# Kernel optimization log

Hardware: AMD Instinct MI355X
Metric: run time of the kernel (lower is better)

Reference implementation:

```python
import jax, jax.numpy as jnp
import numpy as np

EMB_DIM = 1024
ATTN_DIM = 1024


def setup_inputs() -> dict:
    key = jax.random.key(0)
    k_x, k_wk, k_wq, k_wv = jax.random.split(key, 4)
    bound = 1.0 / np.sqrt(EMB_DIM)  # nn.Linear default init range
    return {
        "embedded": jax.random.normal(k_x, (4, 2048, EMB_DIM), dtype=jnp.float32),
        "W_k": jax.random.uniform(k_wk, (ATTN_DIM, EMB_DIM), jnp.float32, -bound, bound),
        "W_q": jax.random.uniform(k_wq, (ATTN_DIM, EMB_DIM), jnp.float32, -bound, bound),
        "W_v": jax.random.uniform(k_wv, (ATTN_DIM, EMB_DIM), jnp.float32, -bound, bound),
    }


def reference(embedded, W_k, W_q, W_v):
    # Linear (bias=False): y = x @ W.T
    K = jnp.einsum("bse,ae->bsa", embedded, W_k)
    Q = jnp.einsum("bse,ae->bsa", embedded, W_q)
    V = jnp.einsum("bse,ae->bsa", embedded, W_v)
    S = K.shape[1]
    scale = 1.0 / jnp.sqrt(jnp.float32(ATTN_DIM))
    scores = jnp.einsum("bqa,bka->bqk", Q, K) * scale  # [B, S, S]
    causal = jnp.tril(jnp.ones((S, S), dtype=bool))  # True = keep
    scores = jnp.where(causal[None, :, :], scores, -jnp.inf)
    attn = jax.nn.softmax(scores, axis=2)
    out = jnp.einsum("bqk,bka->bqa", attn, V)
    # torch.round(x, decimals=4)
    return jnp.round(out * 1e4) / 1e4
```

## Files before the change

### kernel.cpp

```cpp
#include <hip/hip_runtime.h>
#include <stdint.h>

#define B_ 4
#define S_ 2048
#define E_ 1024
#define D_ 1024

typedef short  bf16x8 __attribute__((ext_vector_type(8)));
typedef float  f32x4  __attribute__((ext_vector_type(4)));

static __device__ __forceinline__ unsigned short f2bf(float f) {
    unsigned int u = __float_as_uint(f);
    u += 0x7fffu + ((u >> 16) & 1u);
    return (unsigned short)(u >> 16);
}

static __device__ __forceinline__ void async16(const unsigned short* g, unsigned short* l) {
    auto gp = (const __attribute__((address_space(1))) void*)(uintptr_t)g;
    auto lp = (__attribute__((address_space(3))) void*)(uintptr_t)l;
    __builtin_amdgcn_global_load_lds(gp, lp, 16, 0, 0);
}


__global__ __launch_bounds__(256)
void convert_kernel(const float* __restrict__ x,  const float* __restrict__ Wk,
                    const float* __restrict__ Wq, const float* __restrict__ Wv,
                    unsigned short* __restrict__ xb, unsigned short* __restrict__ Wb)
{
    const long long total  = (long long)B_ * S_ * E_ + 3LL * D_ * E_;
    const long long stride = (long long)gridDim.x * 256 * 4;
    for (long long idx = ((long long)blockIdx.x * 256 + threadIdx.x) * 4;
         idx < total; idx += stride) {
        const float* src; unsigned short* dst; long long off;
        if (idx < (long long)B_ * S_ * E_) {
            src = x; dst = xb; off = idx;
        } else {
            long long w = idx - (long long)B_ * S_ * E_;
            const int sel = (int)(w >> 20);
            off = w & 1048575LL;
            src = (sel == 0) ? Wk : (sel == 1) ? Wq : Wv;
            dst = Wb + ((long long)sel << 20);
        }
        const float4 f = *(const float4*)(src + off);
        ushort4 u = { f2bf(f.x), f2bf(f.y), f2bf(f.z), f2bf(f.w) };
        *(ushort4*)(dst + off) = u;
    }
}

__global__ __launch_bounds__(512, 2)
void proj_kernel(const unsigned short* __restrict__ xb,
                 const unsigned short* __restrict__ Wb,
                 unsigned short* __restrict__ Qb,
                 unsigned short* __restrict__ Kb,
                 unsigned short* __restrict__ Vt)
{
    extern __shared__ __align__(16) unsigned short lds[];

    const int bid = blockIdx.x;
    const int swz = (bid & 7) * 48 + (bid >> 3);
    const int my  = swz / 12;
    const int ny  = swz - my * 12;
    const int m0  = my * 256;
    const int wsel = ny >> 2;
    const int nloc = (ny & 3) * 256;

    const int t = threadIdx.x;
    const int lane = t & 63, wave = t >> 6;
    const int l15 = lane & 15, quad = lane >> 4;
    const int wm2 = wave & 1, wn4 = wave >> 1;
    const int lr = lane >> 3;
    const int lc = ((lane & 7) ^ lr) * 8;
    const int l7 = l15 & 7;

    const unsigned short* gAb = xb + (size_t)(m0 + lr) * E_ + lc;
    const unsigned short* gBb = Wb + (size_t)(ny * 256 + lr) * E_ + lc;

    f32x4 acc[8][4];
    #pragma unroll
    for (int i = 0; i < 8; i++)
        #pragma unroll
        for (int j = 0; j < 4; j++) acc[i][j] = {0.f, 0.f, 0.f, 0.f};

    #pragma unroll
    for (int i = 0; i < 8; i++) {
        const int u = wave * 8 + i;
        if (u < 32) async16(gAb + (size_t)(u * 8) * E_,        lds +         u * 512);
        else        async16(gBb + (size_t)((u - 32) * 8) * E_, lds + 32768 + (u - 32) * 512);
    }
    __syncthreads();

    for (int kt = 0; kt < 16; kt++) {
        const int c = kt & 1;
        const unsigned short* Ac = lds + c * 16384;
        const unsigned short* Bc = lds + 32768 + c * 16384;
        unsigned short* An = lds + (c ^ 1) * 16384;
        unsigned short* Bn = lds + 32768 + (c ^ 1) * 16384;

        #pragma unroll
        for (int p = 0; p < 4; p++) {
            if (kt < 15) {
                const int k0 = (kt + 1) * 64;
                #pragma unroll
                for (int i = 0; i < 2; i++) {
                    const int u = wave * 8 + p * 2 + i;
                    if (u < 32) async16(gAb + (size_t)(u * 8) * E_ + k0,        An +        u * 512);
                    else        async16(gBb + (size_t)((u - 32) * 8) * E_ + k0, Bn + (u - 32) * 512);
                }
            }
            const int mh = p >> 1, nh = p & 1;
            bf16x8 af[2][4], bfr[2][2];
            #pragma unroll
            for (int s = 0; s < 2; s++) {
                const int cs = ((s * 4 + quad) ^ l7) * 8;
                #pragma unroll
                for (int ii = 0; ii < 4; ii++) {
                    const int r = wm2 * 128 + (mh * 4 + ii) * 16 + l15;
                    af[s][ii] = *(const bf16x8*)&Ac[r * 64 + cs];
                }
                #pragma unroll
                for (int jj = 0; jj < 2; jj++) {
                    const int r = wn4 * 64 + (nh * 2 + jj) * 16 + l15;
                    bfr[s][jj] = *(const bf16x8*)&Bc[r * 64 + cs];
                }
            }
            __builtin_amdgcn_s_setprio(1);
            #pragma unroll
            for (int s = 0; s < 2; s++)
                #pragma unroll
                for (int ii = 0; ii < 4; ii++)
                    #pragma unroll
                    for (int jj = 0; jj < 2; jj++)
                        acc[mh * 4 + ii][nh * 2 + jj] =
                            __builtin_amdgcn_mfma_f32_16x16x32_bf16(
                                af[s][ii], bfr[s][jj], acc[mh * 4 + ii][nh * 2 + jj], 0, 0, 0);
            __builtin_amdgcn_s_setprio(0);
            if (p < 3) __builtin_amdgcn_s_barrier();
        }
        __syncthreads();
    }

    if (wsel == 0) {
        #pragma unroll
        for (int i = 0; i < 8; i++)
            #pragma unroll
            for (int j = 0; j < 4; j++) {
                const int gn = nloc + wn4 * 64 + j * 16 + l15;
                #pragma unroll
                for (int r = 0; r < 4; r++) {
                    const int gm = m0 + wm2 * 128 + i * 16 + quad * 4 + r;
                    Kb[(size_t)gm * D_ + gn] = f2bf(acc[i][j][r]);
                }
            }
    } else if (wsel == 1) {
        #pragma unroll
        for (int i = 0; i < 8; i++)
            #pragma unroll
            for (int j = 0; j < 4; j++) {
                const int gn = nloc + wn4 * 64 + j * 16 + l15;
                #pragma unroll
                for (int r = 0; r < 4; r++) {
                    const int gm = m0 + wm2 * 128 + i * 16 + quad * 4 + r;
                    Qb[(size_t)gm * D_ + gn] = f2bf(acc[i][j][r] * 0.03125f);
                }
            }
    } else {
        #pragma unroll
        for (int i = 0; i < 8; i++)
            #pragma unroll
            for (int j = 0; j < 4; j++) {
                const int s0 = m0 + wm2 * 128 + i * 16 + quad * 4;
                const int b  = s0 >> 11, sl = s0 & (S_ - 1);
                const int gn = nloc + wn4 * 64 + j * 16 + l15;
                ushort4 u = { f2bf(acc[i][j][0]), f2bf(acc[i][j][1]),
                              f2bf(acc[i][j][2]), f2bf(acc[i][j][3]) };
                *(ushort4*)&Vt[((size_t)(b << 10) + gn) * S_ + sl] = u;
            }
    }
}

__global__ __launch_bounds__(256, 4)
void expscores_kernel(const unsigned short* __restrict__ Qb,
                      const unsigned short* __restrict__ Kb,
                      unsigned short* __restrict__ P,
                      float* __restrict__ rowpart)
{
    int rem = blockIdx.x;
    int mt = 15, cnt = 16;
    while (rem >= cnt) { rem -= cnt; mt--; cnt--; }
    const int nt = rem;
    const int b  = blockIdx.y;

    __shared__ __align__(16) unsigned short As[128 * 64];
    __shared__ __align__(16) unsigned short Bs[128 * 64];

    const int t = threadIdx.x;
    const int m0 = mt * 128, n0 = nt * 128;

    const int lane = t & 63, wave = t >> 6;
    const int l15 = lane & 15, quad = lane >> 4;
    const int wm = wave & 1, wn = wave >> 1;
    const int sr = lane >> 3;
    const int sq = ((lane & 7) ^ sr) * 8;
    const int l7 = l15 & 7;

    const unsigned short* gA = Qb + (size_t)b * S_ * D_ + (size_t)(m0 + wave * 32 + sr) * D_ + sq;
    const unsigned short* gB = Kb + (size_t)b * S_ * D_ + (size_t)(n0 + wave * 32 + sr) * D_ + sq;
    unsigned short* lA = &As[wave * 2048];
    unsigned short* lB = &Bs[wave * 2048];

    f32x4 acc[4][4];
    #pragma unroll
    for (int i = 0; i < 4; i++)
        #pragma unroll
        for (int j = 0; j < 4; j++) acc[i][j] = {0.f, 0.f, 0.f, 0.f};

    for (int kt = 0; kt < 16; kt++) {
        const int k0 = kt * 64;
        __syncthreads();
        #pragma unroll
        for (int i = 0; i < 4; i++) {
            async16(gA + k0 + i * 8 * D_, lA + i * 512);
            async16(gB + k0 + i * 8 * D_, lB + i * 512);
        }
        __syncthreads();

        #pragma unroll
        for (int s = 0; s < 2; s++) {
            const int cs = ((s * 4 + quad) ^ l7) * 8;
            bf16x8 af[4], bfr[4];
            #pragma unroll
            for (int i = 0; i < 4; i++)
                af[i] = *(const bf16x8*)&As[(wm * 64 + i * 16 + l15) * 64 + cs];
            #pragma unroll
            for (int j = 0; j < 4; j++)
                bfr[j] = *(const bf16x8*)&Bs[(wn * 64 + j * 16 + l15) * 64 + cs];
            #pragma unroll
            for (int i = 0; i < 4; i++)
                #pragma unroll
                for (int j = 0; j < 4; j++)
                    acc[i][j] = __builtin_amdgcn_mfma_f32_16x16x32_bf16(af[i], bfr[j], acc[i][j], 0, 0, 0);
        }
    }

    unsigned short* Pb = P + (size_t)b * S_ * S_;
    #pragma unroll
    for (int i = 0; i < 4; i++)
        #pragma unroll
        for (int j = 0; j < 4; j++) {
            const int gn = n0 + wn * 64 + j * 16 + l15;
            #pragma unroll
            for (int r = 0; r < 4; r++) {
                const int gm = m0 + wm * 64 + i * 16 + quad * 4 + r;
                const float e = (gn <= gm) ? __expf(acc[i][j][r]) : 0.f;
                acc[i][j][r] = e;
                Pb[(size_t)gm * S_ + gn] = f2bf(e);
            }
        }

    float* rp = rowpart + ((size_t)b * 32 + nt * 2 + wn) * S_;
    #pragma unroll
    for (int i = 0; i < 4; i++) {
        float rsub[4];
        #pragma unroll
        for (int r = 0; r < 4; r++) {
            float s = acc[i][0][r] + acc[i][1][r] + acc[i][2][r] + acc[i][3][r];
            #pragma unroll
            for (int off = 8; off; off >>= 1) s += __shfl_xor(s, off);
            rsub[r] = s;
        }
        if (l15 == 0) {
            #pragma unroll
            for (int r = 0; r < 4; r++)
                rp[m0 + wm * 64 + i * 16 + quad * 4 + r] = rsub[r];
        }
    }
}

__global__ __launch_bounds__(256, 2)
void pv_kernel(const unsigned short* __restrict__ P,
               const unsigned short* __restrict__ Vt,
               const float* __restrict__ rowpart,
               float* __restrict__ out)
{
    const int nt = blockIdx.x;
    const int yy = blockIdx.y;
    const int b  = blockIdx.z;
    const int mt = (b & 2) ? yy : (15 - yy);

    __shared__ __align__(16) unsigned short As[2 * 128 * 64];
    __shared__ __align__(16) unsigned short Bs[2 * 128 * 64];

    const int t = threadIdx.x;
    const int m0 = mt * 128, n0 = nt * 128;
    const int niter = 2 * mt + 2;

    const int lane = t & 63, wave = t >> 6;
    const int l15 = lane & 15, quad = lane >> 4;
    const int wm = wave & 1, wn = wave >> 1;
    const int sr = lane >> 3;
    const int sq = ((lane & 7) ^ sr) * 8;
    const int l7 = l15 & 7;

    const unsigned short* gA = P  + (size_t)b * S_ * S_ + (size_t)(m0 + wave * 32 + sr) * S_ + sq;
    const unsigned short* gB = Vt + (size_t)b * D_ * S_ + (size_t)(n0 + wave * 32 + sr) * S_ + sq;
    unsigned short* lA = &As[wave * 2048];
    unsigned short* lB = &Bs[wave * 2048];

    const float* rp = rowpart + (size_t)b * 32 * S_ + (m0 + wm * 64 + lane);
    float rsum = 0.f;
    for (int k = 0; k < niter; k++) rsum += rp[(size_t)k * S_];
    const float invr = 1.0f / rsum;

    f32x4 acc[4][4];
    #pragma unroll
    for (int i = 0; i < 4; i++)
        #pragma unroll
        for (int j = 0; j < 4; j++) acc[i][j] = {0.f, 0.f, 0.f, 0.f};

    #pragma unroll
    for (int i = 0; i < 4; i++) {
        async16(gA + i * 8 * S_, lA + i * 512);
        async16(gB + i * 8 * S_, lB + i * 512);
    }

    int buf = 0;
    for (int kt = 0; kt < niter; kt++) {
        __syncthreads();
        if (kt + 1 < niter) {
            const int k0 = (kt + 1) * 64;
            const int nb = (buf ^ 1) * 8192;
            #pragma unroll
            for (int i = 0; i < 4; i++) {
                async16(gA + k0 + i * 8 * S_, lA + nb + i * 512);
                async16(gB + k0 + i * 8 * S_, lB + nb + i * 512);
            }
        }
        const unsigned short* Ac = As + buf * 8192;
        const unsigned short* Bc = Bs + buf * 8192;
        #pragma unroll
        for (int s = 0; s < 2; s++) {
            const int cs = ((s * 4 + quad) ^ l7) * 8;
            bf16x8 af[4], bfr[4];
            #pragma unroll
            for (int i = 0; i < 4; i++)
                af[i] = *(const bf16x8*)&Ac[(wm * 64 + i * 16 + l15) * 64 + cs];
            #pragma unroll
            for (int j = 0; j < 4; j++)
                bfr[j] = *(const bf16x8*)&Bc[(wn * 64 + j * 16 + l15) * 64 + cs];
            #pragma unroll
            for (int i = 0; i < 4; i++)
                #pragma unroll
                for (int j = 0; j < 4; j++)
                    acc[i][j] = __builtin_amdgcn_mfma_f32_16x16x32_bf16(af[i], bfr[j], acc[i][j], 0, 0, 0);
        }
        buf ^= 1;
    }

    #pragma unroll
    for (int i = 0; i < 4; i++) {
        #pragma unroll
        for (int r = 0; r < 4; r++) {
            const float vr = __shfl(invr, i * 16 + quad * 4 + r);
            const int gm = m0 + wm * 64 + i * 16 + quad * 4 + r;
            #pragma unroll
            for (int j = 0; j < 4; j++) {
                const int gn = n0 + wn * 64 + j * 16 + l15;
                out[((size_t)b * S_ + gm) * D_ + gn] = rintf(acc[i][j][r] * vr * 1e4f) * 1e-4f;
            }
        }
    }
}

extern "C" void kernel_launch(void* const* d_in, const int* in_sizes, int n_in,
                              void* d_out, int out_size, void* d_ws, size_t ws_size,
                              hipStream_t stream)
{
    (void)in_sizes; (void)n_in; (void)out_size; (void)ws_size;
    const float* x  = (const float*)d_in[0];
    const float* Wk = (const float*)d_in[1];
    const float* Wq = (const float*)d_in[2];
    const float* Wv = (const float*)d_in[3];
    float* out = (float*)d_out;

    char* ws = (char*)d_ws;
    unsigned short* Qb = (unsigned short*)ws;
    unsigned short* Kb = Qb + (size_t)B_ * S_ * D_;
    unsigned short* Vt = Kb + (size_t)B_ * S_ * D_;
    unsigned short* P  = Vt + (size_t)B_ * D_ * S_;
    unsigned short* xb = P;
    unsigned short* Wb = xb + (size_t)B_ * S_ * E_;
    float* rowpart = (float*)(P + (size_t)B_ * S_ * S_);

    convert_kernel  <<<2048, 256, 0, stream>>>(x, Wk, Wq, Wv, xb, Wb);
    proj_kernel     <<<dim3(384, 1, 1), 512, 131072, stream>>>(xb, Wb, Qb, Kb, Vt);
    expscores_kernel<<<dim3(136, B_, 1), 256, 0, stream>>>(Qb, Kb, P, rowpart);
    pv_kernel       <<<dim3(8, 16, B_),  256, 0, stream>>>(P, Vt, rowpart, out);
}
```

Measured before the change: 238.1 us.

## Restructure QKV projection GEMM into 256x128 tiles with triple-buffered async loads

Result: faster. 229.5 us (-3.6%).

```diff
diff --git a/kernel.cpp b/kernel.cpp
--- a/kernel.cpp
+++ b/kernel.cpp
@@ -57,12 +57,12 @@
     extern __shared__ __align__(16) unsigned short lds[];
 
     const int bid = blockIdx.x;
-    const int swz = (bid & 7) * 48 + (bid >> 3);
-    const int my  = swz / 12;
-    const int ny  = swz - my * 12;
-    const int m0  = my * 256;
-    const int wsel = ny >> 2;
-    const int nloc = (ny & 3) * 256;
+    const int xcd = bid & 7, ii = bid >> 3;
+    const int my = xcd * 4 + ii / 24;
+    const int ny = ii % 24;
+    const int m0 = my * 256;
+    const int wsel = ny >> 3;
+    const int nloc = (ny & 7) * 128;
 
     const int t = threadIdx.x;
     const int lane = t & 63, wave = t >> 6;
@@ -72,107 +72,136 @@
     const int lc = ((lane & 7) ^ lr) * 8;
     const int l7 = l15 & 7;
 
-    const unsigned short* gAb = xb + (size_t)(m0 + lr) * E_ + lc;
-    const unsigned short* gBb = Wb + (size_t)(ny * 256 + lr) * E_ + lc;
-
-    f32x4 acc[8][4];
+    const unsigned short* gA = xb + (size_t)(m0 + lr) * E_ + lc;
+    const unsigned short* gB = Wb + (size_t)(ny * 128 + lr) * E_ + lc;
+    const int uA = wave * 4;
+    const int uB = wave * 2;
+
+    f32x4 acc[8][2];
     #pragma unroll
     for (int i = 0; i < 8; i++)
         #pragma unroll
-        for (int j = 0; j < 4; j++) acc[i][j] = {0.f, 0.f, 0.f, 0.f};
-
-    #pragma unroll
-    for (int i = 0; i < 8; i++) {
-        const int u = wave * 8 + i;
-        if (u < 32) async16(gAb + (size_t)(u * 8) * E_,        lds +         u * 512);
-        else        async16(gBb + (size_t)((u - 32) * 8) * E_, lds + 32768 + (u - 32) * 512);
-    }
-    __syncthreads();
-
+        for (int j = 0; j < 2; j++) acc[i][j] = {0.f, 0.f, 0.f, 0.f};
+
+    #pragma unroll
+    for (int j = 0; j < 4; j++) async16(gA + (size_t)((uA + j) * 8) * E_, lds + (uA + j) * 512);
+    #pragma unroll
+    for (int j = 0; j < 2; j++) async16(gB + (size_t)((uB + j) * 8) * E_, lds + 49152 + (uB + j) * 512);
+    #pragma unroll
+    for (int j = 0; j < 4; j++) async16(gA + (size_t)((uA + j) * 8) * E_ + 64, lds + 16384 + (uA + j) * 512);
+    #pragma unroll
+    for (int j = 0; j < 2; j++) async16(gB + (size_t)((uB + j) * 8) * E_ + 64, lds + 49152 + 8192 + (uB + j) * 512);
+    asm volatile("s_waitcnt vmcnt(6)" ::: "memory");
+    __builtin_amdgcn_s_barrier();
+
+    int cbuf = 0;
     for (int kt = 0; kt < 16; kt++) {
-        const int c = kt & 1;
-        const unsigned short* Ac = lds + c * 16384;
-        const unsigned short* Bc = lds + 32768 + c * 16384;
-        unsigned short* An = lds + (c ^ 1) * 16384;
-        unsigned short* Bn = lds + 32768 + (c ^ 1) * 16384;
-
-        #pragma unroll
-        for (int p = 0; p < 4; p++) {
-            if (kt < 15) {
-                const int k0 = (kt + 1) * 64;
-                #pragma unroll
-                for (int i = 0; i < 2; i++) {
-                    const int u = wave * 8 + p * 2 + i;
-                    if (u < 32) async16(gAb + (size_t)(u * 8) * E_ + k0,        An +        u * 512);
-                    else        async16(gBb + (size_t)((u - 32) * 8) * E_ + k0, Bn + (u - 32) * 512);
+        const unsigned short* Ac = lds + cbuf * 16384;
+        const unsigned short* Bc = lds + 49152 + cbuf * 8192;
+        const int sbuf = (cbuf >= 1) ? (cbuf - 1) : 2;
+        unsigned short* An = lds + sbuf * 16384;
+        unsigned short* Bn = lds + 49152 + sbuf * 8192;
+        const int k0n = (kt + 2) * 64;
+        const bool st = (kt < 14);
+
+        if (st) {
+            async16(gA + (size_t)((uA + 0) * 8) * E_ + k0n, An + (uA + 0) * 512);
+            async16(gA + (size_t)((uA + 1) * 8) * E_ + k0n, An + (uA + 1) * 512);
+            async16(gA + (size_t)((uA + 2) * 8) * E_ + k0n, An + (uA + 2) * 512);
+        }
+        bf16x8 af[4][2], bfv[2][2];
+        #pragma unroll
+        for (int s = 0; s < 2; s++) {
+            const int cs = ((s * 4 + quad) ^ l7) * 8;
+            #pragma unroll
+            for (int mf = 0; mf < 4; mf++)
+                af[mf][s] = *(const bf16x8*)&Ac[(wm2 * 128 + mf * 16 + l15) * 64 + cs];
+            #pragma unroll
+            for (int nf = 0; nf < 2; nf++)
+                bfv[nf][s] = *(const bf16x8*)&Bc[(wn4 * 32 + nf * 16 + l15) * 64 + cs];
+        }
+        __builtin_amdgcn_s_barrier();
+        asm volatile("s_waitcnt lgkmcnt(0)" ::: "memory");
+        __builtin_amdgcn_sched_barrier(0);
+        __builtin_amdgcn_s_setprio(1);
+        #pragma unroll
+        for (int s = 0; s < 2; s++)
+            #pragma unroll
+            for (int mf = 0; mf < 4; mf++)
+                #pragma unroll
+                for (int nf = 0; nf < 2; nf++)
+                    acc[mf][nf] = __builtin_amdgcn_mfma_f32_16x16x32_bf16(
+                        af[mf][s], bfv[nf][s], acc[mf][nf], 0, 0, 0);
+        __builtin_amdgcn_s_setprio(0);
+        __builtin_amdgcn_s_barrier();
+
+        if (st) {
+            async16(gA + (size_t)((uA + 3) * 8) * E_ + k0n, An + (uA + 3) * 512);
+            async16(gB + (size_t)((uB + 0) * 8) * E_ + k0n, Bn + (uB + 0) * 512);
+            async16(gB + (size_t)((uB + 1) * 8) * E_ + k0n, Bn + (uB + 1) * 512);
+        }
+        bf16x8 ag[4][2];
+        #pragma unroll
+        for (int s = 0; s < 2; s++) {
+            const int cs = ((s * 4 + quad) ^ l7) * 8;
+            #pragma unroll
+            for (int mf = 0; mf < 4; mf++)
+                ag[mf][s] = *(const bf16x8*)&Ac[(wm2 * 128 + (4 + mf) * 16 + l15) * 64 + cs];
+        }
+        __builtin_amdgcn_s_barrier();
+        asm volatile("s_waitcnt lgkmcnt(0)" ::: "memory");
+        __builtin_amdgcn_sched_barrier(0);
+        __builtin_amdgcn_s_setprio(1);
+        #pragma unroll
+        for (int s = 0; s < 2; s++)
+            #pragma unroll
+            for (int mf = 0; mf < 4; mf++)
+                #pragma unroll
+                for (int nf = 0; nf < 2; nf++)
+                    acc[4 + mf][nf] = __builtin_amdgcn_mfma_f32_16x16x32_bf16(
+                        ag[mf][s], bfv[nf][s], acc[4 + mf][nf], 0, 0, 0);
+        __builtin_amdgcn_s_setprio(0);
+
+        if (st) asm volatile("s_waitcnt vmcnt(6)" ::: "memory");
+        else    asm volatile("s_waitcnt vmcnt(0)" ::: "memory");
+        __builtin_amdgcn_s_barrier();
+        cbuf = (cbuf >= 2) ? 0 : cbuf + 1;
+    }
+
+    if (wsel == 0) {
+        #pragma unroll
+        for (int mf = 0; mf < 8; mf++)
+            #pragma unroll
+            for (int nf = 0; nf < 2; nf++) {
+                const int gn = nloc + wn4 * 32 + nf * 16 + l15;
+                #pragma unroll
+                for (int r = 0; r < 4; r++) {
+                    const int gm = m0 + wm2 * 128 + mf * 16 + quad * 4 + r;
+                    Kb[(size_t)gm * D_ + gn] = f2bf(acc[mf][nf][r]);
                 }
             }
-            const int mh = p >> 1, nh = p & 1;
-            bf16x8 af[2][4], bfr[2][2];
-            #pragma unroll
-            for (int s = 0; s < 2; s++) {
-                const int cs = ((s * 4 + quad) ^ l7) * 8;
-                #pragma unroll
-                for (int ii = 0; ii < 4; ii++) {
-                    const int r = wm2 * 128 + (mh * 4 + ii) * 16 + l15;
-                    af[s][ii] = *(const bf16x8*)&Ac[r * 64 + cs];
+    } else if (wsel == 1) {
+        #pragma unroll
+        for (int mf = 0; mf < 8; mf++)
+            #pragma unroll
+            for (int nf = 0; nf < 2; nf++) {
+                const int gn = nloc + wn4 * 32 + nf * 16 + l15;
+                #pragma unroll
+                for (int r = 0; r < 4; r++) {
+                    const int gm = m0 + wm2 * 128 + mf * 16 + quad * 4 + r;
+                    Qb[(size_t)gm * D_ + gn] = f2bf(acc[mf][nf][r] * 0.03125f);
                 }
-                #pragma unroll
-                for (int jj = 0; jj < 2; jj++) {
-                    const int r = wn4 * 64 + (nh * 2 + jj) * 16 + l15;
-                    bfr[s][jj] = *(const bf16x8*)&Bc[r * 64 + cs];
-                }
-            }
-            __builtin_amdgcn_s_setprio(1);
-            #pragma unroll
-            for (int s = 0; s < 2; s++)
-                #pragma unroll
-                for (int ii = 0; ii < 4; ii++)
-                    #pragma unroll
-                    for (int jj = 0; jj < 2; jj++)
-                        acc[mh * 4 + ii][nh * 2 + jj] =
-                            __builtin_amdgcn_mfma_f32_16x16x32_bf16(
-                                af[s][ii], bfr[s][jj], acc[mh * 4 + ii][nh * 2 + jj], 0, 0, 0);
-            __builtin_amdgcn_s_setprio(0);
-            if (p < 3) __builtin_amdgcn_s_barrier();
-        }
-        __syncthreads();
-    }
-
-    if (wsel == 0) {
-        #pragma unroll
-        for (int i = 0; i < 8; i++)
-            #pragma unroll
-            for (int j = 0; j < 4; j++) {
-                const int gn = nloc + wn4 * 64 + j * 16 + l15;
-                #pragma unroll
-                for (int r = 0; r < 4; r++) {
-                    const int gm = m0 + wm2 * 128 + i * 16 + quad * 4 + r;
-                    Kb[(size_t)gm * D_ + gn] = f2bf(acc[i][j][r]);
-                }
-            }
-    } else if (wsel == 1) {
-        #pragma unroll
-        for (int i = 0; i < 8; i++)
-            #pragma unroll
-            for (int j = 0; j < 4; j++) {
-                const int gn = nloc + wn4 * 64 + j * 16 + l15;
-                #pragma unroll
-                for (int r = 0; r < 4; r++) {
-                    const int gm = m0 + wm2 * 128 + i * 16 + quad * 4 + r;
-                    Qb[(size_t)gm * D_ + gn] = f2bf(acc[i][j][r] * 0.03125f);
-                }
             }
     } else {
         #pragma unroll
-        for (int i = 0; i < 8; i++)
-            #pragma unroll
-            for (int j = 0; j < 4; j++) {
-                const int s0 = m0 + wm2 * 128 + i * 16 + quad * 4;
+        for (int mf = 0; mf < 8; mf++)
+            #pragma unroll
+            for (int nf = 0; nf < 2; nf++) {
+                const int s0 = m0 + wm2 * 128 + mf * 16 + quad * 4;
                 const int b  = s0 >> 11, sl = s0 & (S_ - 1);
-                const int gn = nloc + wn4 * 64 + j * 16 + l15;
-                ushort4 u = { f2bf(acc[i][j][0]), f2bf(acc[i][j][1]),
-                              f2bf(acc[i][j][2]), f2bf(acc[i][j][3]) };
+                const int gn = nloc + wn4 * 32 + nf * 16 + l15;
+                ushort4 u = { f2bf(acc[mf][nf][0]), f2bf(acc[mf][nf][1]),
+                              f2bf(acc[mf][nf][2]), f2bf(acc[mf][nf][3]) };
                 *(ushort4*)&Vt[((size_t)(b << 10) + gn) * S_ + sl] = u;
             }
     }
@@ -392,7 +421,7 @@
     float* rowpart = (float*)(P + (size_t)B_ * S_ * S_);
 
     convert_kernel  <<<2048, 256, 0, stream>>>(x, Wk, Wq, Wv, xb, Wb);
-    proj_kernel     <<<dim3(384, 1, 1), 512, 131072, stream>>>(xb, Wb, Qb, Kb, Vt);
+    proj_kernel     <<<dim3(768, 1, 1), 512, 147456, stream>>>(xb, Wb, Qb, Kb, Vt);
     expscores_kernel<<<dim3(136, B_, 1), 256, 0, stream>>>(Qb, Kb, P, rowpart);
     pv_kernel       <<<dim3(8, 16, B_),  256, 0, stream>>>(P, Vt, rowpart, out);
 }
```
